# Performance work log

Hardware: AMD Instinct MI355X
Metric: run time of the kernel (lower is better)

The kernel has to match this reference:

```python
import jax, jax.numpy as jnp
import numpy as np

# Static pyramid shapes (H, W) per level; must match setup_inputs().
SPATIAL_SHAPES = [(128, 128), (64, 64), (32, 32), (16, 16)]
N, LQ, D_MODEL, M, L, P = 2, 21760, 256, 8, 4, 4
D_HEAD = D_MODEL // M
LEN_IN = sum(h * w for h, w in SPATIAL_SHAPES)


def _bilinear_sample(v, grid, H, W):
    """torch.grid_sample(mode=bilinear, padding=zeros, align_corners=False).
    v: [B, H, W, D], grid: [B, Q, P, 2] (x, y) in [-1, 1] -> [B, Q, P, D]."""
    gx = (grid[..., 0] + 1.0) * (W * 0.5) - 0.5
    gy = (grid[..., 1] + 1.0) * (H * 0.5) - 0.5
    x0 = jnp.floor(gx)
    y0 = jnp.floor(gy)
    wx1 = gx - x0
    wy1 = gy - y0
    b = jnp.arange(v.shape[0])[:, None, None]

    def gather(yi, xi):
        valid = (xi >= 0) & (xi <= W - 1) & (yi >= 0) & (yi <= H - 1)
        xc = jnp.clip(xi, 0, W - 1).astype(jnp.int32)
        yc = jnp.clip(yi, 0, H - 1).astype(jnp.int32)
        return v[b, yc, xc] * valid[..., None].astype(v.dtype)

    return (gather(y0, x0) * ((1 - wy1) * (1 - wx1))[..., None]
            + gather(y0, x0 + 1) * ((1 - wy1) * wx1)[..., None]
            + gather(y0 + 1, x0) * (wy1 * (1 - wx1))[..., None]
            + gather(y0 + 1, x0 + 1) * (wy1 * wx1)[..., None])


def setup_inputs() -> dict:
    key = jax.random.key(0)
    ks = jax.random.split(key, 12)
    s = 0.02
    return {
        "query": jax.random.normal(ks[0], (N, LQ, D_MODEL), jnp.float32),
        "reference_points": jax.random.uniform(ks[1], (N, LQ, L, 2), jnp.float32),
        "value": jax.random.normal(ks[2], (N, LEN_IN, D_MODEL), jnp.float32),
        "value_spatial_shapes": jnp.array(SPATIAL_SHAPES, jnp.int32),
        "W_val": jax.random.normal(ks[3], (D_MODEL, D_MODEL), jnp.float32) * s,
        "b_val": jnp.zeros((D_MODEL,), jnp.float32),
        "W_off": jax.random.normal(ks[4], (D_MODEL, M * L * P * 2), jnp.float32) * s,
        "b_off": jax.random.normal(ks[5], (M * L * P * 2,), jnp.float32) * s,
        "W_attn": jax.random.normal(ks[6], (D_MODEL, M * L * P), jnp.float32) * s,
        "b_attn": jnp.zeros((M * L * P,), jnp.float32),
        "W_out": jax.random.normal(ks[7], (D_MODEL, D_MODEL), jnp.float32) * s,
        "b_out": jnp.zeros((D_MODEL,), jnp.float32),
    }


def reference(query, reference_points, value, value_spatial_shapes,
              W_val, b_val, W_off, b_off, W_attn, b_attn, W_out, b_out):
    # value_spatial_shapes is treated as static (SPATIAL_SHAPES) for jit safety.
    v = (value @ W_val + b_val).reshape(N, LEN_IN, M, D_HEAD)
    off = (query @ W_off + b_off).reshape(N, LQ, M, L, P, 2)
    aw = jax.nn.softmax((query @ W_attn + b_attn).reshape(N, LQ, M, L * P), axis=-1)
    aw = aw.reshape(N, LQ, M, L, P)
    # normalizer stacks (W, H) -> x normalized by W, y by H
    norm = jnp.array([[w, h] for h, w in SPATIAL_SHAPES], dtype=query.dtype)
    loc = reference_points[:, :, None, :, None, :] + off / norm[None, None, None, :, None, :]
    grid = 2.0 * loc - 1.0  # [N, LQ, M, L, P, 2]

    out = jnp.zeros((N * M, LQ, D_HEAD), query.dtype)
    start = 0
    for lid, (H, W) in enumerate(SPATIAL_SHAPES):
        vl = v[:, start:start + H * W].reshape(N, H, W, M, D_HEAD)
        vl = vl.transpose(0, 3, 1, 2, 4).reshape(N * M, H, W, D_HEAD)
        gl = grid[:, :, :, lid].transpose(0, 2, 1, 3, 4).reshape(N * M, LQ, P, 2)
        sl = _bilinear_sample(vl, gl, H, W)  # [N*M, LQ, P, D]
        wl = aw[:, :, :, lid].transpose(0, 2, 1, 3).reshape(N * M, LQ, P)
        out = out + jnp.einsum('bqpd,bqp->bqd', sl, wl)
        start += H * W

    out = out.reshape(N, M, LQ, D_HEAD).transpose(0, 2, 1, 3).reshape(N, LQ, D_MODEL)
    return out @ W_out + b_out
```

## Files before the change

kernel.cpp:

```cpp
#include <hip/hip_runtime.h>

typedef __attribute__((ext_vector_type(8))) short short8;
typedef __attribute__((ext_vector_type(4))) float floatx4;

#define N_    2
#define LQ_   21760
#define D_    256
#define M_    8
#define L_    4
#define P_    4
#define DH_   32
#define LEN_  21760
#define BQ    16

__constant__ int c_start[4] = {0, 16384, 20480, 21504};
__constant__ int c_HW[4]    = {128, 64, 32, 16};

#define WT_BYTE_OFF 22282240u

__device__ __forceinline__ unsigned short f2bf(float f) {
  unsigned int u = __builtin_bit_cast(unsigned int, f);
  u += 0x7fffu + ((u >> 16) & 1u);
  return (unsigned short)(u >> 16);
}

__global__ __launch_bounds__(256) void prep_kernel(
    const float* __restrict__ Woff, const float* __restrict__ Watt,
    const float* __restrict__ Wout, const float* __restrict__ Wv,
    unsigned short* __restrict__ wt) {
  const int b = blockIdx.x, t = threadIdx.x;
  const float* src; int ncols, n; unsigned short* dst;
  if (b < 256)      { src = Woff; ncols = 256; n = b;       dst = wt + 0      + n * 256; }
  else if (b < 384) { src = Watt; ncols = 128; n = b - 256; dst = wt + 65536  + n * 256; }
  else if (b < 640) { src = Wout; ncols = 256; n = b - 384; dst = wt + 98304  + n * 256; }
  else              { src = Wv;   ncols = 256; n = b - 640; dst = wt + 163840 + n * 256; }
  dst[t] = f2bf(src[(size_t)t * ncols + n]);
}

__global__ __launch_bounds__(256, 2) void vproj_kernel(
    const float* __restrict__ value, const unsigned short* __restrict__ Wvt,
    const float* __restrict__ bv, unsigned short* __restrict__ vout) {
  __shared__ unsigned short vs[64][264];
  const int t = threadIdx.x;
  const int r0 = blockIdx.x * 64;
  {
    const int c2 = (t & 127) * 2;
    const int rb = t >> 7;
#pragma unroll
    for (int i = 0; i < 32; ++i) {
      int rr = rb + i * 2;
      float2 v = *(const float2*)(value + (size_t)(r0 + rr) * D_ + c2);
      *(unsigned int*)&vs[rr][c2] = (unsigned int)f2bf(v.x) | ((unsigned int)f2bf(v.y) << 16);
    }
  }
  __syncthreads();
  const int wave = t >> 6, lane = t & 63;
  const int arow = wave * 16 + (lane & 15);
  const int kg = (lane >> 4) * 8;
  floatx4 acc[16] = {};
  for (int kk = 0; kk < 8; ++kk) {
    const int k0 = kk * 32;
    short8 af = *(const short8*)&vs[arow][k0 + kg];
#pragma unroll
    for (int ct = 0; ct < 16; ++ct) {
      const int col = ct * 16 + (lane & 15);
      short8 bf = *(const short8*)(Wvt + col * 256 + k0 + kg);
      acc[ct] = __builtin_amdgcn_mfma_f32_16x16x32_bf16(af, bf, acc[ct], 0, 0, 0);
    }
  }
  const int n = (r0 >= LEN_) ? 1 : 0;
  const int pixbase = r0 - n * LEN_ + wave * 16 + ((lane >> 4) * 4);
#pragma unroll
  for (int ct = 0; ct < 16; ++ct) {
    const int gc = ct * 16 + (lane & 15);
    const int m = gc >> 5, d = gc & 31;
    const float bb = bv[gc];
    unsigned short* ob = vout + ((size_t)(n * M_ + m) * LEN_) * DH_ + d;
#pragma unroll
    for (int j = 0; j < 4; ++j)
      ob[(size_t)(pixbase + j) * DH_] = f2bf(acc[ct][j] + bb);
  }
}

__global__ __launch_bounds__(256, 4) void msda_kernel(
    const float* __restrict__ query, const float* __restrict__ refp,
    const unsigned short* __restrict__ wt,
    const float* __restrict__ boff, const float* __restrict__ batt,
    const float* __restrict__ bout,
    const unsigned short* __restrict__ vproj, float* __restrict__ out) {
  __shared__ unsigned short qs[BQ][264];
  __shared__ float oa[BQ][388];
  __shared__ short idxs[2][128][4];
  __shared__ float wls[2][128][4];

  const int t = threadIdx.x;
  const int qg0 = blockIdx.x * BQ;
  const int n = qg0 / LQ_;

  {
    const int c2 = (t & 127) * 2;
    const int rb = t >> 7;
#pragma unroll
    for (int i = 0; i < 8; ++i) {
      int rr = rb + i * 2;
      float2 v = *(const float2*)(query + (size_t)(qg0 + rr) * D_ + c2);
      *(unsigned int*)&qs[rr][c2] = (unsigned int)f2bf(v.x) | ((unsigned int)f2bf(v.y) << 16);
    }
  }
  __syncthreads();

  const int wave = t >> 6, lane = t & 63;
  const int arow = lane & 15;
  const int kg = (lane >> 4) * 8;
  const int row0 = (lane >> 4) * 4;

  {
    floatx4 acc[6] = {};
    for (int kk = 0; kk < 8; ++kk) {
      const int k0 = kk * 32;
      short8 af = *(const short8*)&qs[arow][k0 + kg];
#pragma unroll
      for (int i = 0; i < 6; ++i) {
        const int col = wave * 96 + i * 16 + (lane & 15);
        const unsigned short* bp = (col < 256) ? (wt + col * 256)
                                               : (wt + 65536 + (col - 256) * 256);
        short8 bf = *(const short8*)(bp + k0 + kg);
        acc[i] = __builtin_amdgcn_mfma_f32_16x16x32_bf16(af, bf, acc[i], 0, 0, 0);
      }
    }
#pragma unroll
    for (int i = 0; i < 6; ++i) {
      const int col = wave * 96 + i * 16 + (lane & 15);
      const float bb = (col < 256) ? boff[col] : batt[col - 256];
#pragma unroll
      for (int j = 0; j < 4; ++j) oa[row0 + j][col] = acc[i][j] + bb;
    }
  }
  __syncthreads();

  if (t < 128) {
    const int q = t >> 3, m = t & 7;
    float v[16]; float mx = -1e30f;
#pragma unroll
    for (int s = 0; s < 16; ++s) { v[s] = oa[q][256 + m * 16 + s]; mx = fmaxf(mx, v[s]); }
    float sum = 0.f;
#pragma unroll
    for (int s = 0; s < 16; ++s) { v[s] = __expf(v[s] - mx); sum += v[s]; }
    const float inv = 1.f / sum;
#pragma unroll
    for (int s = 0; s < 16; ++s) oa[q][256 + m * 16 + s] = v[s] * inv;
  }
  __syncthreads();

  const int m_g = t >> 5;
  const int g = t & 31;
  const int p8 = g >> 3;
  const int d4 = (g & 7) * 4;
  const unsigned short* vbase = vproj + ((size_t)(n * M_ + m_g) * LEN_) * DH_ + d4;

  for (int q = 0; q < BQ; ++q) {
    const int slot = q & 1;
    if (t < 128) {
      const int l = (t >> 2) & 3;
      const int Wl = c_HW[l];
      const int st = c_start[l];
      const float rx = refp[(((size_t)(qg0 + q)) * L_ + l) * 2 + 0];
      const float ry = refp[(((size_t)(qg0 + q)) * L_ + l) * 2 + 1];
      const float gx = rx * (float)Wl + oa[q][2 * t]     - 0.5f;
      const float gy = ry * (float)Wl + oa[q][2 * t + 1] - 0.5f;
      const float fx0 = floorf(gx), fy0 = floorf(gy);
      const int x0 = (int)fx0, y0 = (int)fy0;
      const float wx1 = gx - fx0, wy1 = gy - fy0;
      const float wx0 = 1.f - wx1, wy0 = 1.f - wy1;
      const float a = oa[q][256 + t];
      const bool vx0 = (x0 >= 0) && (x0 < Wl);
      const bool vx1 = (x0 + 1 >= 0) && (x0 + 1 < Wl);
      const bool vy0 = (y0 >= 0) && (y0 < Wl);
      const bool vy1 = (y0 + 1 >= 0) && (y0 + 1 < Wl);
      idxs[slot][t][0] = (short)((vx0 && vy0) ? st + y0 * Wl + x0 : -1);
      idxs[slot][t][1] = (short)((vx1 && vy0) ? st + y0 * Wl + x0 + 1 : -1);
      idxs[slot][t][2] = (short)((vx0 && vy1) ? st + (y0 + 1) * Wl + x0 : -1);
      idxs[slot][t][3] = (short)((vx1 && vy1) ? st + (y0 + 1) * Wl + x0 + 1 : -1);
      wls[slot][t][0] = wy0 * wx0 * a;
      wls[slot][t][1] = wy0 * wx1 * a;
      wls[slot][t][2] = wy1 * wx0 * a;
      wls[slot][t][3] = wy1 * wx1 * a;
    }
    __syncthreads();

    float a0 = 0.f, a1 = 0.f, a2 = 0.f, a3 = 0.f;
    const int sidb = m_g * 16;
#pragma unroll
    for (int s = 0; s < 16; ++s) {
      const int ix = (int)idxs[slot][sidb + s][p8];
      const int ixc = (ix >= 0) ? ix : 0;
      const float wv = (ix >= 0) ? wls[slot][sidb + s][p8] : 0.f;
      const unsigned short* p = vbase + (size_t)ixc * DH_;
      const uint2 u = *(const uint2*)p;
      a0 += __builtin_bit_cast(float, u.x << 16) * wv;
      a1 += __builtin_bit_cast(float, u.x & 0xffff0000u) * wv;
      a2 += __builtin_bit_cast(float, u.y << 16) * wv;
      a3 += __builtin_bit_cast(float, u.y & 0xffff0000u) * wv;
    }
    a0 += __shfl_xor(a0, 8);  a1 += __shfl_xor(a1, 8);
    a2 += __shfl_xor(a2, 8);  a3 += __shfl_xor(a3, 8);
    a0 += __shfl_xor(a0, 16); a1 += __shfl_xor(a1, 16);
    a2 += __shfl_xor(a2, 16); a3 += __shfl_xor(a3, 16);
    if (g < 8) {
      unsigned int* mp = (unsigned int*)&qs[q][m_g * 32 + d4];
      mp[0] = (unsigned int)f2bf(a0) | ((unsigned int)f2bf(a1) << 16);
      mp[1] = (unsigned int)f2bf(a2) | ((unsigned int)f2bf(a3) << 16);
    }
  }
  __syncthreads();

  {
    floatx4 acc[4] = {};
    for (int kk = 0; kk < 8; ++kk) {
      const int k0 = kk * 32;
      short8 af = *(const short8*)&qs[arow][k0 + kg];
#pragma unroll
      for (int i = 0; i < 4; ++i) {
        const int col = wave * 64 + i * 16 + (lane & 15);
        short8 bf = *(const short8*)(wt + 98304 + col * 256 + k0 + kg);
        acc[i] = __builtin_amdgcn_mfma_f32_16x16x32_bf16(af, bf, acc[i], 0, 0, 0);
      }
    }
#pragma unroll
    for (int i = 0; i < 4; ++i) {
      const int col = wave * 64 + i * 16 + (lane & 15);
      const float bb = bout[col];
#pragma unroll
      for (int j = 0; j < 4; ++j)
        out[(size_t)(qg0 + row0 + j) * D_ + col] = acc[i][j] + bb;
    }
  }
}

extern "C" void kernel_launch(void* const* d_in, const int* in_sizes, int n_in,
                              void* d_out, int out_size, void* d_ws, size_t ws_size,
                              hipStream_t stream) {
  const float* query = (const float*)d_in[0];
  const float* refp  = (const float*)d_in[1];
  const float* value = (const float*)d_in[2];
  const float* Wv    = (const float*)d_in[4];
  const float* bv    = (const float*)d_in[5];
  const float* Woff  = (const float*)d_in[6];
  const float* boff  = (const float*)d_in[7];
  const float* Watt  = (const float*)d_in[8];
  const float* batt  = (const float*)d_in[9];
  const float* Wout  = (const float*)d_in[10];
  const float* bout  = (const float*)d_in[11];
  float* out = (float*)d_out;

  unsigned short* vproj = (unsigned short*)d_ws;
  unsigned short* wt    = (unsigned short*)((char*)d_ws + WT_BYTE_OFF);
  const unsigned short* Wvt = wt + 163840;

  dim3 blk(256);
  hipLaunchKernelGGL(prep_kernel, dim3(896), blk, 0, stream, Woff, Watt, Wout, Wv, wt);
  hipLaunchKernelGGL(vproj_kernel, dim3((N_ * LEN_) / 64), blk, 0, stream, value, Wvt, bv, vproj);
  hipLaunchKernelGGL(msda_kernel, dim3((N_ * LQ_) / BQ), blk, 0, stream,
                     query, refp, wt, boff, batt, bout, vproj, out);
}
```

Baseline: 269.3 us.

## Process two queries per sampling iteration and store offsets as bf16 in LDS

The sampling loop now handles two queries per iteration. All 256 threads compute bilinear indices and weights (two queries at once instead of only 128 threads for one), which halves the number of barriers and doubles the independent gathers in flight per thread. The sampling offsets are stored in shared memory as bf16 rather than fp32, which shrinks LDS use and may allow higher occupancy. The cost is lower precision in the sampling locations, which could move sample coordinates on the finer pyramid levels, plus more registers for the second accumulator set.

```diff
diff --git a/kernel.cpp b/kernel.cpp
--- a/kernel.cpp
+++ b/kernel.cpp
@@ -22,6 +22,9 @@
   unsigned int u = __builtin_bit_cast(unsigned int, f);
   u += 0x7fffu + ((u >> 16) & 1u);
   return (unsigned short)(u >> 16);
+}
+__device__ __forceinline__ float bf2f(unsigned short s) {
+  return __builtin_bit_cast(float, ((unsigned int)s) << 16);
 }
 
 __global__ __launch_bounds__(256) void prep_kernel(
@@ -89,9 +92,10 @@
     const float* __restrict__ bout,
     const unsigned short* __restrict__ vproj, float* __restrict__ out) {
   __shared__ unsigned short qs[BQ][264];
-  __shared__ float oa[BQ][388];
-  __shared__ short idxs[2][128][4];
-  __shared__ float wls[2][128][4];
+  __shared__ unsigned short offb[BQ][256];
+  __shared__ float awb[BQ][128];
+  __shared__ short idxs[4][128][4];
+  __shared__ float wls[4][128][4];
 
   const int t = threadIdx.x;
   const int qg0 = blockIdx.x * BQ;
@@ -131,9 +135,15 @@
 #pragma unroll
     for (int i = 0; i < 6; ++i) {
       const int col = wave * 96 + i * 16 + (lane & 15);
-      const float bb = (col < 256) ? boff[col] : batt[col - 256];
-#pragma unroll
-      for (int j = 0; j < 4; ++j) oa[row0 + j][col] = acc[i][j] + bb;
+      if (col < 256) {
+        const float bb = boff[col];
+#pragma unroll
+        for (int j = 0; j < 4; ++j) offb[row0 + j][col] = f2bf(acc[i][j] + bb);
+      } else {
+        const float bb = batt[col - 256];
+#pragma unroll
+        for (int j = 0; j < 4; ++j) awb[row0 + j][col - 256] = acc[i][j] + bb;
+      }
     }
   }
   __syncthreads();
@@ -142,59 +152,64 @@
     const int q = t >> 3, m = t & 7;
     float v[16]; float mx = -1e30f;
 #pragma unroll
-    for (int s = 0; s < 16; ++s) { v[s] = oa[q][256 + m * 16 + s]; mx = fmaxf(mx, v[s]); }
+    for (int s = 0; s < 16; ++s) { v[s] = awb[q][m * 16 + s]; mx = fmaxf(mx, v[s]); }
     float sum = 0.f;
 #pragma unroll
     for (int s = 0; s < 16; ++s) { v[s] = __expf(v[s] - mx); sum += v[s]; }
     const float inv = 1.f / sum;
 #pragma unroll
-    for (int s = 0; s < 16; ++s) oa[q][256 + m * 16 + s] = v[s] * inv;
-  }
-  __syncthreads();
-
+    for (int s = 0; s < 16; ++s) awb[q][m * 16 + s] = v[s] * inv;
+  }
+  __syncthreads();
+
+  const int sid = t & 127;
+  const int qh  = t >> 7;
   const int m_g = t >> 5;
   const int g = t & 31;
   const int p8 = g >> 3;
   const int d4 = (g & 7) * 4;
   const unsigned short* vbase = vproj + ((size_t)(n * M_ + m_g) * LEN_) * DH_ + d4;
 
-  for (int q = 0; q < BQ; ++q) {
-    const int slot = q & 1;
-    if (t < 128) {
-      const int l = (t >> 2) & 3;
+  for (int e = 0; e < 8; ++e) {
+    const int qp = 2 * e + qh;
+    const int slot = qp & 3;
+    {
+      const int l = (sid >> 2) & 3;
       const int Wl = c_HW[l];
       const int st = c_start[l];
-      const float rx = refp[(((size_t)(qg0 + q)) * L_ + l) * 2 + 0];
-      const float ry = refp[(((size_t)(qg0 + q)) * L_ + l) * 2 + 1];
-      const float gx = rx * (float)Wl + oa[q][2 * t]     - 0.5f;
-      const float gy = ry * (float)Wl + oa[q][2 * t + 1] - 0.5f;
+      const float rx = refp[(((size_t)(qg0 + qp)) * L_ + l) * 2 + 0];
+      const float ry = refp[(((size_t)(qg0 + qp)) * L_ + l) * 2 + 1];
+      const float gx = rx * (float)Wl + bf2f(offb[qp][2 * sid])     - 0.5f;
+      const float gy = ry * (float)Wl + bf2f(offb[qp][2 * sid + 1]) - 0.5f;
       const float fx0 = floorf(gx), fy0 = floorf(gy);
       const int x0 = (int)fx0, y0 = (int)fy0;
       const float wx1 = gx - fx0, wy1 = gy - fy0;
       const float wx0 = 1.f - wx1, wy0 = 1.f - wy1;
-      const float a = oa[q][256 + t];
+      const float a = awb[qp][sid];
       const bool vx0 = (x0 >= 0) && (x0 < Wl);
       const bool vx1 = (x0 + 1 >= 0) && (x0 + 1 < Wl);
       const bool vy0 = (y0 >= 0) && (y0 < Wl);
       const bool vy1 = (y0 + 1 >= 0) && (y0 + 1 < Wl);
-      idxs[slot][t][0] = (short)((vx0 && vy0) ? st + y0 * Wl + x0 : -1);
-      idxs[slot][t][1] = (short)((vx1 && vy0) ? st + y0 * Wl + x0 + 1 : -1);
-      idxs[slot][t][2] = (short)((vx0 && vy1) ? st + (y0 + 1) * Wl + x0 : -1);
-      idxs[slot][t][3] = (short)((vx1 && vy1) ? st + (y0 + 1) * Wl + x0 + 1 : -1);
-      wls[slot][t][0] = wy0 * wx0 * a;
-      wls[slot][t][1] = wy0 * wx1 * a;
-      wls[slot][t][2] = wy1 * wx0 * a;
-      wls[slot][t][3] = wy1 * wx1 * a;
+      idxs[slot][sid][0] = (short)((vx0 && vy0) ? st + y0 * Wl + x0 : -1);
+      idxs[slot][sid][1] = (short)((vx1 && vy0) ? st + y0 * Wl + x0 + 1 : -1);
+      idxs[slot][sid][2] = (short)((vx0 && vy1) ? st + (y0 + 1) * Wl + x0 : -1);
+      idxs[slot][sid][3] = (short)((vx1 && vy1) ? st + (y0 + 1) * Wl + x0 + 1 : -1);
+      wls[slot][sid][0] = wy0 * wx0 * a;
+      wls[slot][sid][1] = wy0 * wx1 * a;
+      wls[slot][sid][2] = wy1 * wx0 * a;
+      wls[slot][sid][3] = wy1 * wx1 * a;
     }
     __syncthreads();
 
+    const int sl0 = (2 * e) & 3, sl1 = sl0 + 1;
+    const int sidb = m_g * 16;
     float a0 = 0.f, a1 = 0.f, a2 = 0.f, a3 = 0.f;
-    const int sidb = m_g * 16;
+    float b0 = 0.f, b1 = 0.f, b2 = 0.f, b3 = 0.f;
 #pragma unroll
     for (int s = 0; s < 16; ++s) {
-      const int ix = (int)idxs[slot][sidb + s][p8];
+      const int ix = (int)idxs[sl0][sidb + s][p8];
       const int ixc = (ix >= 0) ? ix : 0;
-      const float wv = (ix >= 0) ? wls[slot][sidb + s][p8] : 0.f;
+      const float wv = (ix >= 0) ? wls[sl0][sidb + s][p8] : 0.f;
       const unsigned short* p = vbase + (size_t)ixc * DH_;
       const uint2 u = *(const uint2*)p;
       a0 += __builtin_bit_cast(float, u.x << 16) * wv;
@@ -202,14 +217,33 @@
       a2 += __builtin_bit_cast(float, u.y << 16) * wv;
       a3 += __builtin_bit_cast(float, u.y & 0xffff0000u) * wv;
     }
+#pragma unroll
+    for (int s = 0; s < 16; ++s) {
+      const int ix = (int)idxs[sl1][sidb + s][p8];
+      const int ixc = (ix >= 0) ? ix : 0;
+      const float wv = (ix >= 0) ? wls[sl1][sidb + s][p8] : 0.f;
+      const unsigned short* p = vbase + (size_t)ixc * DH_;
+      const uint2 u = *(const uint2*)p;
+      b0 += __builtin_bit_cast(float, u.x << 16) * wv;
+      b1 += __builtin_bit_cast(float, u.x & 0xffff0000u) * wv;
+      b2 += __builtin_bit_cast(float, u.y << 16) * wv;
+      b3 += __builtin_bit_cast(float, u.y & 0xffff0000u) * wv;
+    }
     a0 += __shfl_xor(a0, 8);  a1 += __shfl_xor(a1, 8);
     a2 += __shfl_xor(a2, 8);  a3 += __shfl_xor(a3, 8);
     a0 += __shfl_xor(a0, 16); a1 += __shfl_xor(a1, 16);
     a2 += __shfl_xor(a2, 16); a3 += __shfl_xor(a3, 16);
+    b0 += __shfl_xor(b0, 8);  b1 += __shfl_xor(b1, 8);
+    b2 += __shfl_xor(b2, 8);  b3 += __shfl_xor(b3, 8);
+    b0 += __shfl_xor(b0, 16); b1 += __shfl_xor(b1, 16);
+    b2 += __shfl_xor(b2, 16); b3 += __shfl_xor(b3, 16);
     if (g < 8) {
-      unsigned int* mp = (unsigned int*)&qs[q][m_g * 32 + d4];
-      mp[0] = (unsigned int)f2bf(a0) | ((unsigned int)f2bf(a1) << 16);
-      mp[1] = (unsigned int)f2bf(a2) | ((unsigned int)f2bf(a3) << 16);
+      unsigned int* mp0 = (unsigned int*)&qs[2 * e][m_g * 32 + d4];
+      mp0[0] = (unsigned int)f2bf(a0) | ((unsigned int)f2bf(a1) << 16);
+      mp0[1] = (unsigned int)f2bf(a2) | ((unsigned int)f2bf(a3) << 16);
+      unsigned int* mp1 = (unsigned int*)&qs[2 * e + 1][m_g * 32 + d4];
+      mp1[0] = (unsigned int)f2bf(b0) | ((unsigned int)f2bf(b1) << 16);
+      mp1[1] = (unsigned int)f2bf(b2) | ((unsigned int)f2bf(b3) << 16);
     }
   }
   __syncthreads();
```

Result: slower. 313.8 us (+16.5%).
